# Performance work log

Measured on AMD Instinct MI355X. Metric: run time of the kernel, lower is better.

## Reference

```python
import jax, jax.numpy as jnp
import numpy as np

H = 16          # num_heads
D = 64          # head_dim = dim // num_heads
ROPE_THETA = 10000.0
NEG = -1e9


def _rope_angles(n, d):
    # matches get_1d_rotary_pos_embed(head_dim, N): freqs_cis = polar(1, t outer (theta^-(2i/d)))
    inv_freq = 1.0 / (ROPE_THETA ** (jnp.arange(0, d, 2, dtype=jnp.float32) / d))  # [d/2]
    ang = jnp.arange(n, dtype=jnp.float32)[:, None] * inv_freq[None, :]            # [n, d/2]
    return jnp.cos(ang), jnp.sin(ang)


def _apply_rope(x, cos, sin):
    # x: [B,H,N,D]; complex rotation on adjacent pairs (use_real=False semantics)
    x0 = x[..., 0::2]
    x1 = x[..., 1::2]
    # broadcast cos/sin [N, D/2] over batch and heads
    r0 = x0 * cos - x1 * sin
    r1 = x0 * sin + x1 * cos
    return jnp.stack([r0, r1], axis=-1).reshape(x.shape)


def setup_inputs() -> dict:
    key = jax.random.key(0)
    ks = jax.random.split(key, 5)
    B, N, C = 4, 2048, 1024
    s_in = 1.0 / np.sqrt(C)
    return {
        "x": jax.random.normal(ks[0], (B, N, C), dtype=jnp.float32),
        "Wqkv_w": jax.random.normal(ks[1], (3 * C, C), dtype=jnp.float32) * s_in,
        "Wqkv_b": jax.random.normal(ks[2], (3 * C,), dtype=jnp.float32) * 0.01,
        "out_w": jax.random.normal(ks[3], (C, C), dtype=jnp.float32) * s_in,
        "out_b": jax.random.normal(ks[4], (C,), dtype=jnp.float32) * 0.01,
    }


def reference(x, Wqkv_w, Wqkv_b, out_w, out_b):
    B, N, C = x.shape
    scale = D ** -0.5
    # fused QKV projection: [B,N,3C] -> [3,B,H,N,D]
    qkv = (jnp.einsum('bnc,oc->bno', x, Wqkv_w) + Wqkv_b)
    qkv = qkv.reshape(B, N, 3, H, D).transpose(2, 0, 3, 1, 4)
    q, k, v = qkv[0], qkv[1], qkv[2]
    # qk_norm=False -> Identity
    cos, sin = _rope_angles(N, D)
    q = _apply_rope(q, cos, sin)
    k = _apply_rope(k, cos, sin)
    attn = jnp.einsum('bhqd,bhkd->bhqk', q * scale, k)      # [B,H,N,N]
    causal = jnp.triu(jnp.ones((N, N), dtype=bool), k=1)
    attn = jnp.where(causal[None, None], NEG, attn)
    attn = jax.nn.softmax(attn, axis=-1)
    o = jnp.einsum('bhqk,bhkd->bhqd', attn, v)              # [B,H,N,D]
    o = o.transpose(0, 2, 1, 3).reshape(B, N, C)
    return jnp.einsum('bnc,oc->bno', o, out_w) + out_b
```

## Files before the change

kernel.cpp:

```cpp
#include <hip/hip_runtime.h>
#include <hip/hip_bf16.h>

#define DEVI __device__ __forceinline__

typedef __attribute__((ext_vector_type(8))) short short8v;
typedef __attribute__((ext_vector_type(4))) float f32x4;
typedef __attribute__((ext_vector_type(16))) float f32x16;
typedef __attribute__((ext_vector_type(2))) unsigned u32x2;
typedef __attribute__((ext_vector_type(4))) unsigned u32x4;

DEVI short f2bf(float f) {
  __hip_bfloat16 h = __float2bfloat16(f);
  return __builtin_bit_cast(short, h);
}
DEVI float bf2f(short s) {
  unsigned u = ((unsigned)(unsigned short)s) << 16;
  return __builtin_bit_cast(float, u);
}
DEVI unsigned packbf(float a, float b) {
  return (unsigned)(unsigned short)f2bf(a) | ((unsigned)(unsigned short)f2bf(b) << 16);
}
DEVI void gload16(const void* g, void* l) {
  __builtin_amdgcn_global_load_lds((const __attribute__((address_space(1))) void*)g,
                                   (__attribute__((address_space(3))) void*)l, 16, 0, 0);
}
#define MFMA16(a, b, c) __builtin_amdgcn_mfma_f32_16x16x32_bf16((a), (b), (c), 0, 0, 0)
#define MFMA32(a, b, c) __builtin_amdgcn_mfma_f32_32x32x16_bf16((a), (b), (c), 0, 0, 0)
#define PLSWAP(a, b) asm("v_permlane32_swap_b32 %0, %1" : "+v"(a), "+v"(b))


__global__ void cvt_all(const float* __restrict__ x, const float* __restrict__ wq,
                        const float* __restrict__ wo, short* __restrict__ xb,
                        short* __restrict__ wqb, short* __restrict__ wob) {
  int i = blockIdx.x * blockDim.x + threadIdx.x;
  const float* in;
  short* out;
  if (i < 2097152) { in = x; out = xb; }
  else if (i < 2097152 + 786432) { in = wq; out = wqb; i -= 2097152; }
  else { in = wo; out = wob; i -= 2097152 + 786432; }
  float4 v = ((const float4*)in)[i];
  short4 o;
  o.x = f2bf(v.x); o.y = f2bf(v.y); o.z = f2bf(v.z); o.w = f2bf(v.w);
  ((short4*)out)[i] = o;
}

__global__ void rope_table(float2* __restrict__ tbl) {
  int i = blockIdx.x * blockDim.x + threadIdx.x;
  int n = i >> 5, f = i & 31;
  float inv = powf(10000.0f, -(float)f * (1.0f / 32.0f));
  float ang = (float)n * inv;
  tbl[i] = make_float2(cosf(ang), sinf(ang));
}

__global__ void rope_k(short* __restrict__ kk, const float2* __restrict__ tbl) {
  int i = blockIdx.x * blockDim.x + threadIdx.x;
  int row = i >> 3, c8 = i & 7;
  int n = row & 2047;
  short* ad = kk + (size_t)row * 64 + c8 * 8;
  short8v vv = *(short8v*)ad;
  short8v ov;
#pragma unroll
  for (int j = 0; j < 4; ++j) {
    float2 cs = tbl[n * 32 + c8 * 4 + j];
    float x0 = bf2f(vv[2 * j]), x1 = bf2f(vv[2 * j + 1]);
    ov[2 * j]     = f2bf(x0 * cs.x - x1 * cs.y);
    ov[2 * j + 1] = f2bf(x0 * cs.y + x1 * cs.x);
  }
  *(short8v*)ad = ov;
}

__global__ __launch_bounds__(512, 2)
void gemm256(const short* __restrict__ A, const short* __restrict__ Bw,
             const float* __restrict__ bias,
             short* __restrict__ q, short* __restrict__ k, short* __restrict__ v,
             int Kdim) {
  __shared__ __attribute__((aligned(16))) short lds[65536];
  const int t = threadIdx.x;
  const int lane = t & 63, w = t >> 6;
  const int wr = w >> 2, wc = w & 3;
  const int g = lane >> 4, r16 = lane & 15;
  const int n0 = blockIdx.x * 256, m0 = blockIdx.y * 256;

  int goffs[4], loffs[4];
#pragma unroll
  for (int p = 0; p < 4; ++p) {
    int c = p * 512 + t;
    int row = c >> 3, u = c & 7;
    goffs[p] = row * Kdim + ((u ^ (row & 7)) * 8);
    loffs[p] = c * 16;
  }
  const short* Abase = A + (size_t)m0 * Kdim;
  const short* Bbase = Bw + (size_t)n0 * Kdim;

  auto STAGE = [&](int s, int k0) {
#pragma unroll
    for (int p = 0; p < 4; ++p) {
      gload16(Abase + k0 + goffs[p], (char*)lds + s * 32768 + loffs[p]);
      gload16(Bbase + k0 + goffs[p], (char*)lds + 65536 + s * 32768 + loffs[p]);
    }
  };

  f32x4 acc[8][4];
#pragma unroll
  for (int i = 0; i < 8; ++i)
#pragma unroll
    for (int j = 0; j < 4; ++j) acc[i][j] = (f32x4){0.f, 0.f, 0.f, 0.f};

  const int nsteps = Kdim >> 6;
  STAGE(0, 0);
  __syncthreads();

  int cur = 0;
  for (int st = 0; st < nsteps; ++st) {
    if (st + 1 < nsteps) STAGE(cur ^ 1, (st + 1) << 6);
    const char* Ab = (const char*)lds + cur * 32768;
    const char* Bb = (const char*)lds + 65536 + cur * 32768;
#pragma unroll
    for (int ks = 0; ks < 2; ++ks) {
      short8v bf[4];
#pragma unroll
      for (int ni = 0; ni < 4; ++ni) {
        int rowb = wc * 64 + ni * 16 + r16;
        bf[ni] = *(const short8v*)(Bb + rowb * 128 + (((ks * 4 + g) ^ (rowb & 7)) << 4));
      }
#pragma unroll
      for (int mi = 0; mi < 8; ++mi) {
        int rowa = wr * 128 + mi * 16 + r16;
        short8v af =
            *(const short8v*)(Ab + rowa * 128 + (((ks * 4 + g) ^ (rowa & 7)) << 4));
#pragma unroll
        for (int ni = 0; ni < 4; ++ni)
          acc[mi][ni] = MFMA16(af, bf[ni], acc[mi][ni]);
      }
    }
    __syncthreads();
    cur ^= 1;
  }

  const int b = m0 >> 11, nb = m0 & 2047;
  if (n0 < 2048) {
#pragma unroll
    for (int ni = 0; ni < 4; ++ni) {
      int col = n0 + wc * 64 + ni * 16 + r16;
      float bv = bias[col];
      int s = col >> 10, h = (col & 1023) >> 6, d = col & 63;
      short* dst = (s == 0) ? q : k;
#pragma unroll
      for (int mi = 0; mi < 8; ++mi) {
        int mrow = m0 + wr * 128 + mi * 16 + g * 4;
#pragma unroll
        for (int r = 0; r < 4; ++r) {
          int n = (mrow + r) & 2047;
          dst[(((size_t)(b * 16 + h)) * 2048 + n) * 64 + d] = f2bf(acc[mi][ni][r] + bv);
        }
      }
    }
  } else {
    short* Cs = lds;
    const int hdrb = (n0 - 2048) >> 6;
#pragma unroll
    for (int hh = 0; hh < 4; ++hh) {
      if (wc == hh) {
#pragma unroll
        for (int ni = 0; ni < 4; ++ni) {
          float bv = bias[n0 + hh * 64 + ni * 16 + r16];
#pragma unroll
          for (int mi = 0; mi < 8; ++mi) {
            u32x2 pk;
            pk[0] = packbf(acc[mi][ni][0] + bv, acc[mi][ni][1] + bv);
            pk[1] = packbf(acc[mi][ni][2] + bv, acc[mi][ni][3] + bv);
            *(u32x2*)&Cs[(ni * 16 + r16) * 264 + wr * 128 + mi * 16 + g * 4] = pk;
          }
        }
      }
      __syncthreads();
      short* vdst = v + ((size_t)(b * 16 + hdrb + hh)) * 64 * 2048;
#pragma unroll
      for (int j = 0; j < 4; ++j) {
        int chunk = j * 512 + t;
        int d = chunk >> 5, c = chunk & 31;
        short8v val = *(const short8v*)&Cs[d * 264 + c * 8];
        *(short8v*)(vdst + (size_t)d * 2048 + nb + c * 8) = val;
      }
      __syncthreads();
    }
  }
}

__global__ __launch_bounds__(256)
void gemm_f32(const short* __restrict__ A, const short* __restrict__ Bw,
              const float* __restrict__ bias, float* __restrict__ fout,
              int Ndim, int Kdim) {
  __shared__ __attribute__((aligned(16))) short As[3][128 * 32];
  __shared__ __attribute__((aligned(16))) short Bs[3][128 * 32];
  const int t = threadIdx.x;
  const int lane = t & 63, w = t >> 6;
  const int wr = w >> 1, wc = w & 1;
  const int g = lane >> 4, r16 = lane & 15;
  const int m0 = blockIdx.y * 128, n0 = blockIdx.x * 128;

  int goffs[2], loffs[2];
#pragma unroll
  for (int p = 0; p < 2; ++p) {
    int c = p * 256 + t;
    int row = c >> 2, u = c & 3;
    goffs[p] = row * Kdim + ((u ^ ((row >> 1) & 3)) * 8);
    loffs[p] = c * 16;
  }
  const short* Abase = A + (size_t)m0 * Kdim;
  const short* Bbase = Bw + (size_t)n0 * Kdim;

  auto STAGE = [&](int s, int k0) {
#pragma unroll
    for (int p = 0; p < 2; ++p) {
      gload16(Abase + k0 + goffs[p], (char*)&As[s][0] + loffs[p]);
      gload16(Bbase + k0 + goffs[p], (char*)&Bs[s][0] + loffs[p]);
    }
  };

  f32x4 acc[4][4];
#pragma unroll
  for (int i = 0; i < 4; ++i)
#pragma unroll
    for (int j = 0; j < 4; ++j) acc[i][j] = (f32x4){0.f, 0.f, 0.f, 0.f};

  const int nsteps = Kdim >> 5;
  STAGE(0, 0);
  STAGE(1, 32);
  asm volatile("s_waitcnt vmcnt(4)" ::: "memory");
  __builtin_amdgcn_s_barrier();
  asm volatile("" ::: "memory");

  int cur = 0, pre = 2;
  const int rsw = (r16 >> 1) & 3;
  for (int st = 0; st < nsteps; ++st) {
    if (st + 2 < nsteps) STAGE(pre, (st + 2) << 5);
    short8v af[4], bf[4];
#pragma unroll
    for (int mi = 0; mi < 4; ++mi)
      af[mi] = *(const short8v*)&As[cur][(wr * 64 + mi * 16 + r16) * 32 +
                                         ((g ^ rsw) * 8)];
#pragma unroll
    for (int ni = 0; ni < 4; ++ni)
      bf[ni] = *(const short8v*)&Bs[cur][(wc * 64 + ni * 16 + r16) * 32 +
                                         ((g ^ rsw) * 8)];
#pragma unroll
    for (int mi = 0; mi < 4; ++mi)
#pragma unroll
      for (int ni = 0; ni < 4; ++ni)
        acc[mi][ni] = MFMA16(af[mi], bf[ni], acc[mi][ni]);
    if (st + 2 < nsteps) asm volatile("s_waitcnt vmcnt(4)" ::: "memory");
    else                 asm volatile("s_waitcnt vmcnt(0)" ::: "memory");
    __builtin_amdgcn_s_barrier();
    asm volatile("" ::: "memory");
    cur = (cur == 2) ? 0 : cur + 1;
    pre = (pre == 2) ? 0 : pre + 1;
  }

#pragma unroll
  for (int ni = 0; ni < 4; ++ni) {
    int col = n0 + wc * 64 + ni * 16 + r16;
    float bv = bias[col];
#pragma unroll
    for (int mi = 0; mi < 4; ++mi) {
      int mrow = m0 + wr * 64 + mi * 16 + g * 4;
#pragma unroll
      for (int r = 0; r < 4; ++r)
        fout[(size_t)(mrow + r) * Ndim + col] = acc[mi][ni][r] + bv;
    }
  }
}

__global__ __launch_bounds__(512)
void fattn(const short* __restrict__ q, const short* __restrict__ k,
           const short* __restrict__ vT, const float2* __restrict__ tbl,
           short* __restrict__ o) {
  const int bx = blockIdx.x;
  const int idx = bx >> 6;
  const int qt = (idx < 4) ? (7 - idx) : (idx - 4);
  const int bh = bx & 63;
  const int b = bh >> 4, h = bh & 15;
  const int t = threadIdx.x, lane = t & 63, w = t >> 6;
  const int q32 = lane & 31, hi = lane >> 5;
  const int hi4 = hi * 4;

  __shared__ __attribute__((aligned(16))) short Ks[2][64 * 64];
  __shared__ __attribute__((aligned(16))) short Vt[2][64 * 64];

  const short* qb = q + (size_t)bh * 2048 * 64;
  const short* kb = k + (size_t)bh * 2048 * 64;
  const short* vb = vT + (size_t)bh * 2048 * 64;

  const int srow = t >> 3, su = t & 7;
  const int sx8 = (su ^ (srow & 7)) * 8;
  const int koff = srow * 64 + sx8;
  const int voff = srow * 2048 + sx8;
  const int loff = t * 16;
  auto STAGE = [&](int s, int kt) {
    gload16(kb + (size_t)kt * 4096 + koff, (char*)&Ks[s][0] + loff);
    gload16(vb + kt * 64 + voff, (char*)&Vt[s][0] + loff);
  };

  const int q0w = qt * 256 + w * 32;
  const int nrow = q0w + q32;

  const float sc = 0.125f * 1.44269504088896f;
  short8v aq[4];
#pragma unroll
  for (int ds = 0; ds < 4; ++ds) {
    short8v raw = *(const short8v*)(qb + (size_t)nrow * 64 + ds * 16 + hi * 8);
    short8v rq;
#pragma unroll
    for (int j = 0; j < 4; ++j) {
      float2 cs = tbl[nrow * 32 + ds * 8 + hi4 + j];
      float x0 = bf2f(raw[2 * j]), x1 = bf2f(raw[2 * j + 1]);
      rq[2 * j]     = f2bf((x0 * cs.x - x1 * cs.y) * sc);
      rq[2 * j + 1] = f2bf((x0 * cs.y + x1 * cs.x) * sc);
    }
    aq[ds] = rq;
  }

  const short one_bf = 0x3F80;
  const short8v ones = {one_bf, one_bf, one_bf, one_bf, one_bf, one_bf, one_bf, one_bf};
  const float M = 24.0f;

  f32x16 oacc[2], lacc;
#pragma unroll
  for (int j = 0; j < 16; ++j) { oacc[0][j] = 0.f; oacc[1][j] = 0.f; lacc[j] = 0.f; }

  const int ktmax = 4 * qt + 3;

  STAGE(0, 0);
  __syncthreads();

  for (int kt = 0; kt <= ktmax; ++kt) {
    const int cur = kt & 1;
    if (kt < ktmax) STAGE(cur ^ 1, kt + 1);

    if (kt * 64 <= q0w + 31) {
      f32x16 s[2];
#pragma unroll
      for (int j = 0; j < 16; ++j) { s[0][j] = 0.f; s[1][j] = 0.f; }
      __builtin_amdgcn_s_setprio(1);
#pragma unroll
      for (int ds = 0; ds < 4; ++ds) {
        int u = 2 * ds + hi;
#pragma unroll
        for (int kbl = 0; kbl < 2; ++kbl) {
          int key = kbl * 32 + q32;
          short8v kf = *(const short8v*)((const char*)&Ks[cur][0] + key * 128 +
                                         ((u ^ (key & 7)) << 4));
          s[kbl] = MFMA32(kf, aq[ds], s[kbl]);
        }
      }
      __builtin_amdgcn_s_setprio(0);

      const bool needmask = (kt * 64 + 63 > q0w);
      unsigned pa[4][4];
#pragma unroll
      for (int kbl = 0; kbl < 2; ++kbl) {
        if (needmask) {
#pragma unroll
          for (int r = 0; r < 16; ++r) {
            int keyg = kt * 64 + kbl * 32 + (r & 3) + 8 * (r >> 2) + hi4;
            if (keyg > nrow) s[kbl][r] = -1e30f;
          }
        }
        unsigned pk[8];
#pragma unroll
        for (int p = 0; p < 8; ++p) {
          float p0 = __builtin_amdgcn_exp2f(s[kbl][2 * p] - M);
          float p1 = __builtin_amdgcn_exp2f(s[kbl][2 * p + 1] - M);
          pk[p] = packbf(p0, p1);
        }
        {
          unsigned x0 = pk[0], x1 = pk[2];
          unsigned y0 = pk[1], y1 = pk[3];
          PLSWAP(x0, x1);
          PLSWAP(y0, y1);
          pa[kbl * 2][0] = x0; pa[kbl * 2][1] = y0;
          pa[kbl * 2][2] = x1; pa[kbl * 2][3] = y1;
        }
        {
          unsigned x0 = pk[4], x1 = pk[6];
          unsigned y0 = pk[5], y1 = pk[7];
          PLSWAP(x0, x1);
          PLSWAP(y0, y1);
          pa[kbl * 2 + 1][0] = x0; pa[kbl * 2 + 1][1] = y0;
          pa[kbl * 2 + 1][2] = x1; pa[kbl * 2 + 1][3] = y1;
        }
      }

      __builtin_amdgcn_s_setprio(1);
#pragma unroll
      for (int kk = 0; kk < 4; ++kk) {
        short8v paf = __builtin_bit_cast(
            short8v, (u32x4){pa[kk][0], pa[kk][1], pa[kk][2], pa[kk][3]});
        lacc = MFMA32(paf, ones, lacc);
        int u = 2 * kk + hi;
#pragma unroll
        for (int db = 0; db < 2; ++db) {
          int d = db * 32 + q32;
          short8v vf = *(const short8v*)((const char*)&Vt[cur][0] + d * 128 +
                                         ((u ^ (d & 7)) << 4));
          oacc[db] = MFMA32(paf, vf, oacc[db]);
        }
      }
      __builtin_amdgcn_s_setprio(0);
    }
    __syncthreads();
  }

#pragma unroll
  for (int r = 0; r < 16; ++r) {
    float ilr = 1.f / lacc[r];
    int qg = q0w + (r & 3) + 8 * (r >> 2) + hi4;
    short* orow = o + ((size_t)(b * 2048 + qg)) * 1024 + h * 64;
    orow[q32]      = f2bf(oacc[0][r] * ilr);
    orow[32 + q32] = f2bf(oacc[1][r] * ilr);
  }
}

extern "C" void kernel_launch(void* const* d_in, const int* in_sizes, int n_in,
                              void* d_out, int out_size, void* d_ws, size_t ws_size,
                              hipStream_t stream) {
  const float* x    = (const float*)d_in[0];
  const float* Wqkv = (const float*)d_in[1];
  const float* bqkv = (const float*)d_in[2];
  const float* Wout = (const float*)d_in[3];
  const float* bout = (const float*)d_in[4];

  char* p = (char*)d_ws;
  short* xb = (short*)p;    p += (size_t)8192 * 1024 * 2;
  short* wqkvb = (short*)p; p += (size_t)3072 * 1024 * 2;
  short* woutb = (short*)p; p += (size_t)1024 * 1024 * 2;
  short* qbf = (short*)p;   p += (size_t)64 * 2048 * 64 * 2;
  short* kbf = (short*)p;   p += (size_t)64 * 2048 * 64 * 2;
  short* vbf = (short*)p;   p += (size_t)64 * 2048 * 64 * 2;
  float2* tbl = (float2*)p; p += (size_t)2048 * 32 * 8;

  cvt_all<<<12288, 256, 0, stream>>>(x, Wqkv, Wout, xb, wqkvb, woutb);
  rope_table<<<256, 256, 0, stream>>>(tbl);

  gemm256<<<dim3(12, 32), 512, 0, stream>>>(xb, wqkvb, bqkv, qbf, kbf, vbf, 1024);
  rope_k<<<4096, 256, 0, stream>>>(kbf, tbl);
  fattn<<<dim3(512), 512, 0, stream>>>(qbf, kbf, vbf, tbl, xb);
  gemm_f32<<<dim3(8, 64), 256, 0, stream>>>(xb, woutb, bout, (float*)d_out, 1024, 1024);
}
```

Before: 183.6 us.

## Interleave QKV GEMM prefetch and MFMA in four quadrant phases

Splits each K step of the QKV projection GEMM into four quadrant phases. Each phase does its LDS fragment loads, issues half-tile global-to-LDS prefetches for the next step and runs its MFMA batch, separated by raw barriers and explicit waitcnts. MFMA sections are raised in priority with s_setprio, and the wait at the end of each step uses per-wave vmcnt thresholds. The aim is to overlap global loads and LDS reads with matrix math better than the single prefetch-then-compute loop did. The per-wave partial vmcnt waits let some waves reach the barrier with their LDS prefetches still in flight, which risks a race on the next buffer. The extra barriers also add sync overhead.

```diff
diff --git a/kernel.cpp b/kernel.cpp
--- a/kernel.cpp
+++ b/kernel.cpp
@@ -81,24 +81,29 @@
   const int g = lane >> 4, r16 = lane & 15;
   const int n0 = blockIdx.x * 256, m0 = blockIdx.y * 256;
 
-  int goffs[4], loffs[4];
-#pragma unroll
-  for (int p = 0; p < 4; ++p) {
+  int goff[2], loff[2];
+#pragma unroll
+  for (int p = 0; p < 2; ++p) {
     int c = p * 512 + t;
     int row = c >> 3, u = c & 7;
-    goffs[p] = row * Kdim + ((u ^ (row & 7)) * 8);
-    loffs[p] = c * 16;
-  }
-  const short* Abase = A + (size_t)m0 * Kdim;
-  const short* Bbase = Bw + (size_t)n0 * Kdim;
-
-  auto STAGE = [&](int s, int k0) {
-#pragma unroll
-    for (int p = 0; p < 4; ++p) {
-      gload16(Abase + k0 + goffs[p], (char*)lds + s * 32768 + loffs[p]);
-      gload16(Bbase + k0 + goffs[p], (char*)lds + 65536 + s * 32768 + loffs[p]);
-    }
+    goff[p] = row * Kdim + ((u ^ (row & 7)) * 8);
+    loff[p] = c * 16;
+  }
+  const short* Ag = A + (size_t)m0 * Kdim;
+  const short* Bg = Bw + (size_t)n0 * Kdim;
+
+  auto STAGE_A = [&](int buf, int k0, int h) {
+#pragma unroll
+    for (int p = 0; p < 2; ++p)
+      gload16(Ag + k0 + h * 128 * Kdim + goff[p],
+              (char*)lds + buf * 32768 + h * 16384 + loff[p]);
   };
+  auto STAGE_B = [&](int buf, int k0, int h) {
+#pragma unroll
+    for (int p = 0; p < 2; ++p)
+      gload16(Bg + k0 + h * 128 * Kdim + goff[p],
+              (char*)lds + 65536 + buf * 32768 + h * 16384 + loff[p]);
+  };
 
   f32x4 acc[8][4];
 #pragma unroll
@@ -106,35 +111,83 @@
 #pragma unroll
     for (int j = 0; j < 4; ++j) acc[i][j] = (f32x4){0.f, 0.f, 0.f, 0.f};
 
+  STAGE_A(0, 0, 0); STAGE_B(0, 0, 0); STAGE_A(0, 0, 1); STAGE_B(0, 0, 1);
+  asm volatile("s_waitcnt vmcnt(0)" ::: "memory");
+  __builtin_amdgcn_s_barrier();
+
   const int nsteps = Kdim >> 6;
-  STAGE(0, 0);
-  __syncthreads();
-
-  int cur = 0;
-  for (int st = 0; st < nsteps; ++st) {
-    if (st + 1 < nsteps) STAGE(cur ^ 1, (st + 1) << 6);
+  for (int kt = 0; kt < nsteps; ++kt) {
+    const int cur = kt & 1;
+    const int knext = (kt + 1) << 6;
+    const bool pf = (kt + 1 < nsteps);
     const char* Ab = (const char*)lds + cur * 32768;
     const char* Bb = (const char*)lds + 65536 + cur * 32768;
-#pragma unroll
-    for (int ks = 0; ks < 2; ++ks) {
-      short8v bf[4];
-#pragma unroll
-      for (int ni = 0; ni < 4; ++ni) {
-        int rowb = wc * 64 + ni * 16 + r16;
-        bf[ni] = *(const short8v*)(Bb + rowb * 128 + (((ks * 4 + g) ^ (rowb & 7)) << 4));
-      }
-#pragma unroll
-      for (int mi = 0; mi < 8; ++mi) {
-        int rowa = wr * 128 + mi * 16 + r16;
-        short8v af =
-            *(const short8v*)(Ab + rowa * 128 + (((ks * 4 + g) ^ (rowa & 7)) << 4));
-#pragma unroll
-        for (int ni = 0; ni < 4; ++ni)
-          acc[mi][ni] = MFMA16(af, bf[ni], acc[mi][ni]);
-      }
-    }
-    __syncthreads();
-    cur ^= 1;
+
+    short8v af[8], bf0[4], bf1[4];
+
+    auto LDA = [&](int mhalf) {
+#pragma unroll
+      for (int mi2 = 0; mi2 < 4; ++mi2) {
+        int row = wr * 128 + (mhalf * 4 + mi2) * 16 + r16;
+#pragma unroll
+        for (int ks = 0; ks < 2; ++ks)
+          af[mi2 * 2 + ks] = *(const short8v*)(Ab + row * 128 +
+                                               (((ks * 4 + g) ^ (row & 7)) << 4));
+      }
+    };
+    auto LDB = [&](short8v* bf, int nhalf) {
+#pragma unroll
+      for (int ni2 = 0; ni2 < 2; ++ni2) {
+        int row = wc * 64 + (nhalf * 2 + ni2) * 16 + r16;
+#pragma unroll
+        for (int ks = 0; ks < 2; ++ks)
+          bf[ni2 * 2 + ks] = *(const short8v*)(Bb + row * 128 +
+                                               (((ks * 4 + g) ^ (row & 7)) << 4));
+      }
+    };
+    auto QUAD = [&](short8v* bf, int mhalf, int nhalf) {
+      __builtin_amdgcn_s_setprio(1);
+#pragma unroll
+      for (int mi2 = 0; mi2 < 4; ++mi2)
+#pragma unroll
+        for (int ni2 = 0; ni2 < 2; ++ni2)
+#pragma unroll
+          for (int ks = 0; ks < 2; ++ks)
+            acc[mhalf * 4 + mi2][nhalf * 2 + ni2] =
+                MFMA16(af[mi2 * 2 + ks], bf[ni2 * 2 + ks],
+                       acc[mhalf * 4 + mi2][nhalf * 2 + ni2]);
+      __builtin_amdgcn_s_setprio(0);
+    };
+
+    LDA(0); LDB(bf0, 0);
+    if (pf) STAGE_A(cur ^ 1, knext, 0);
+    __builtin_amdgcn_s_barrier();
+    asm volatile("s_waitcnt lgkmcnt(0)" ::: "memory");
+    QUAD(bf0, 0, 0);
+    __builtin_amdgcn_s_barrier();
+    LDB(bf1, 1);
+    if (pf) STAGE_B(cur ^ 1, knext, 0);
+    __builtin_amdgcn_s_barrier();
+    asm volatile("s_waitcnt lgkmcnt(0)" ::: "memory");
+    QUAD(bf1, 0, 1);
+    __builtin_amdgcn_s_barrier();
+    LDA(1);
+    if (pf) STAGE_A(cur ^ 1, knext, 1);
+    __builtin_amdgcn_s_barrier();
+    asm volatile("s_waitcnt lgkmcnt(0)" ::: "memory");
+    QUAD(bf0, 1, 0);
+    __builtin_amdgcn_s_barrier();
+    if (pf) STAGE_B(cur ^ 1, knext, 1);
+    __builtin_amdgcn_s_barrier();
+    QUAD(bf1, 1, 1);
+    if (pf) {
+      if (wc >= 2)      asm volatile("s_waitcnt vmcnt(0)" ::: "memory");
+      else if (wr == 1) asm volatile("s_waitcnt vmcnt(2)" ::: "memory");
+      else              asm volatile("s_waitcnt vmcnt(4)" ::: "memory");
+    } else {
+      asm volatile("s_waitcnt vmcnt(0)" ::: "memory");
+    }
+    __builtin_amdgcn_s_barrier();
   }
 
   const int b = m0 >> 11, nb = m0 & 2047;
```

Measured after the change: 189.3 us. 3.1% more time.
